# Kernel optimization log

Measured on AMD Instinct MI355X. Metric: run time of the kernel, lower is better.

The kernel has to match this reference:

```python
import jax, jax.numpy as jnp
import numpy as np

D = 1024       # total one-hot domain width
N = 65536      # number of synthetic records
N_ATTRS = 64   # attributes
BIN = 16       # categories per attribute (equal-size bins: N_ATTRS * BIN == D)
Q = 2048       # number of queries
K = 3          # k-way marginals


def setup_inputs() -> dict:
    key = jax.random.key(0)
    k1, k2 = jax.random.split(key)
    # UnifInitializer: (rand - 0.5) * 2 -> uniform in [-1, 1]
    weight = (jax.random.uniform(k1, (D, N), dtype=jnp.float32) - 0.5) * 2.0
    q_idxs = jax.random.randint(k2, (Q, K), 0, D)  # int query column indices into d
    return {"weight": weight, "q_idxs": q_idxs}


def reference(weight, q_idxs):
    # x = syndata.weight.T : [n, d]
    x = weight.T
    # _get_probs: per-attribute-bin softmax along d. Equal bins -> reshape+softmax.
    probs = jax.nn.softmax(x.reshape(N, N_ATTRS, BIN), axis=-1).reshape(N, D)
    # get_answers: gather query columns, product over k, mean over records.
    gathered = probs[:, q_idxs]          # [n, Q, k]
    answers = gathered.prod(axis=-1).mean(axis=0)  # [Q]
    return answers
```

## Files before the change

### kernel.cpp

```cpp
#include <hip/hip_runtime.h>
#include <stdint.h>

#define D_DIM 1024
#define N_DIM 65536
#define Q_DIM 2048
#define K_DIM 3

#define NBLK  256
#define TPB   1024
#define MACW  32
#define NMAC  8
#define NQT   32
#define QROWS 256

#define RING_OFF  0
#define TAB_OFF   98304
#define LDS_TOTAL 163840

#define VMCNT2() asm volatile("s_waitcnt vmcnt(2)" ::: "memory")
#define VMCNT0() asm volatile("s_waitcnt vmcnt(0)" ::: "memory")
#define LGKM0()  asm volatile("s_waitcnt lgkmcnt(0)" ::: "memory")
#define SCHED0() __builtin_amdgcn_sched_barrier(0)
#define SBAR()   __builtin_amdgcn_s_barrier()

typedef const __attribute__((address_space(1))) uint32_t  glb_u32;
typedef __attribute__((address_space(3))) uint32_t        lds_u32;

__device__ __forceinline__ uint32_t f2bf(float f) {
    uint32_t u = __float_as_uint(f);
    return (u + 0x7fffu + ((u >> 16) & 1u)) >> 16;
}
__device__ __forceinline__ float blo(uint32_t u) { return __uint_as_float(u << 16); }
__device__ __forceinline__ float bhi(uint32_t u) { return __uint_as_float(u & 0xffff0000u); }

__device__ __forceinline__ void stage_quarter(const float* __restrict__ W, char* smem,
                                              int q, int bid, int w, int l) {
    const int slot = (q % 3) * 32768;
    const int col0 = bid * (NMAC * MACW) + (q >> 2) * MACW;
    const int r0   = (q & 3) * QROWS + w * 16 + (l >> 3);
    const float* g0 = W + ((size_t)r0 << 16) + col0 + (l & 7) * 4;
    const float* g1 = W + ((size_t)(r0 + 8) << 16) + col0 + (l & 7) * 4;
    __builtin_amdgcn_global_load_lds((glb_u32*)g0, (lds_u32*)(smem + RING_OFF + slot + w * 2048 + l * 16),        16, 0, 0);
    __builtin_amdgcn_global_lds:
    ;
}

#undef RING_OFF
#define RING_OFF 0

__device__ __forceinline__ void stage_quarter2(const float* __restrict__ W, char* smem,
                                               int q, int bid, int w, int l) {
    const int slot = (q % 3) * 32768;
    const int col0 = bid * (NMAC * MACW) + (q >> 2) * MACW;
    const int r0   = (q & 3) * QROWS + w * 16 + (l >> 3);
    const float* g0 = W + ((size_t)r0 << 16) + col0 + (l & 7) * 4;
    const float* g1 = W + ((size_t)(r0 + 8) << 16) + col0 + (l & 7) * 4;
    __builtin_amdgcn_global_load_lds((glb_u32*)g0,
        (lds_u32*)(smem + RING_OFF + slot + w * 2048 + l * 16), 16, 0, 0);
    __builtin_amdgcn_global_load_lds((glb_u32*)g1,
        (lds_u32*)(smem + RING_OFF + slot + w * 2048 + 1024 + l * 16), 16, 0, 0);
}

#define COMPUTE_PHASE()                                                                           \
    _Pragma("unroll")                                                                             \
    for (int g16 = 0; g16 < 4; ++g16) {                                                           \
        const int gb = g16 << 4;                                                                  \
        {                                                                                         \
            const uint4 va = *(const uint4*)(smem + TAB_OFF + baseb[0][0] + (gb ^ swzb[0][0]));   \
            const uint4 vb = *(const uint4*)(smem + TAB_OFF + baseb[0][1] + (gb ^ swzb[0][1]));   \
            const uint4 vc = *(const uint4*)(smem + TAB_OFF + baseb[0][2] + (gb ^ swzb[0][2]));   \
            acc0 = fmaf(blo(va.x) * blo(vb.x), blo(vc.x), acc0);                                  \
            acc0 = fmaf(bhi(va.x) * bhi(vb.x), bhi(vc.x), acc0);                                  \
            acc0 = fmaf(blo(va.y) * blo(vb.y), blo(vc.y), acc0);                                  \
            acc0 = fmaf(bhi(va.y) * bhi(vb.y), bhi(vc.y), acc0);                                  \
            acc0 = fmaf(blo(va.z) * blo(vb.z), blo(vc.z), acc0);                                  \
            acc0 = fmaf(bhi(va.z) * bhi(vb.z), bhi(vc.z), acc0);                                  \
            acc0 = fmaf(blo(va.w) * blo(vb.w), blo(vc.w), acc0);                                  \
            acc0 = fmaf(bhi(va.w) * bhi(vb.w), bhi(vc.w), acc0);                                  \
        }                                                                                         \
        {                                                                                         \
            const uint4 va = *(const uint4*)(smem + TAB_OFF + baseb[1][0] + (gb ^ swzb[1][0]));   \
            const uint4 vb = *(const uint4*)(smem + TAB_OFF + baseb[1][1] + (gb ^ swzb[1][1]));   \
            const uint4 vc = *(const uint4*)(smem + TAB_OFF + baseb[1][2] + (gb ^ swzb[1][2]));   \
            acc1 = fmaf(blo(va.x) * blo(vb.x), blo(vc.x), acc1);                                  \
            acc1 = fmaf(bhi(va.x) * bhi(vb.x), bhi(vc.x), acc1);                                  \
            acc1 = fmaf(blo(va.y) * blo(vb.y), blo(vc.y), acc1);                                  \
            acc1 = fmaf(bhi(va.y) * bhi(vb.y), bhi(vc.y), acc1);                                  \
            acc1 = fmaf(blo(va.z) * blo(vb.z), blo(vc.z), acc1);                                  \
            acc1 = fmaf(bhi(va.z) * bhi(vb.z), bhi(vc.z), acc1);                                  \
            acc1 = fmaf(blo(va.w) * blo(vb.w), blo(vc.w), acc1);                                  \
            acc1 = fmaf(bhi(va.w) * bhi(vb.w), bhi(vc.w), acc1);                                  \
        }                                                                                         \
    }

template<bool ATOMIC>
__global__ __launch_bounds__(TPB, 4) void rap_main(const float* __restrict__ W,
                                                   const int* __restrict__ qidx,
                                                   float* __restrict__ outp) {
    extern __shared__ char smem[];
    const int tid = threadIdx.x;
    const int bid = blockIdx.x;
    const int w = tid >> 6, l = tid & 63;

    const int q0 = tid * 2;
    int baseb[2][K_DIM];
    int swzb[2][K_DIM];
#pragma unroll
    for (int qq = 0; qq < 2; ++qq) {
#pragma unroll
        for (int k = 0; k < K_DIM; ++k) {
            const int d = qidx[(q0 + qq) * K_DIM + k];
            baseb[qq][k] = d << 6;
            swzb[qq][k]  = ((d >> 1) & 3) << 4;
        }
    }

    const int c = l & 31;
    const int h = l >> 5;

    float acc0 = 0.f, acc1 = 0.f;

    VMCNT0(); SCHED0();
    stage_quarter2(W, smem, 0, bid, w, l);
    stage_quarter2(W, smem, 1, bid, w, l);

    for (int m = 0; m < NMAC; ++m) {
#pragma unroll
        for (int s = 0; s < 4; ++s) {
            const int q = m * 4 + s;
            if (q == NQT - 1) { VMCNT0(); } else { VMCNT2(); }
            SCHED0();

            if (q + 2 < NQT) stage_quarter2(W, smem, q + 2, bid, w, l);
            SCHED0();

            {
                const char* p = smem + RING_OFF + (q % 3) * 32768
                                + (w * 16 + h) * 128 + c * 4;
                float e[8]; float sum = 0.f;
#pragma unroll
                for (int j = 0; j < 8; ++j) {
                    e[j] = __expf(*(const float*)(p + j * 256));
                    sum += e[j];
                }
                sum += __shfl_xor(sum, 32);
                const float rec = __builtin_amdgcn_rcpf(sum);
                const int rbase = s * 256 + w * 16 + h;
#pragma unroll
                for (int j = 0; j < 8; ++j) {
                    const int row = rbase + 2 * j;
                    const uint32_t bf = f2bf(e[j] * rec);
                    *(uint16_t*)(smem + TAB_OFF + row * 64
                                 + ((((c >> 3) ^ ((row >> 1) & 3))) << 4)
                                 + ((c & 7) << 1)) = (uint16_t)bf;
                }
            }
        }

        LGKM0(); SCHED0(); SBAR(); SCHED0();

        COMPUTE_PHASE();

        LGKM0(); SCHED0(); SBAR(); SCHED0();
    }

    if (ATOMIC) {
        atomicAdd(outp + q0,     acc0 * (1.0f / N_DIM));
        atomicAdd(outp + q0 + 1, acc1 * (1.0f / N_DIM));
    } else {
        outp[(size_t)q0 * NBLK + bid]       = acc0;
        outp[(size_t)(q0 + 1) * NBLK + bid] = acc1;
    }
}

__global__ __launch_bounds__(256) void rap_reduce(const float* __restrict__ partials,
                                                  float* __restrict__ outp) {
    const int wv = threadIdx.x >> 6;
    const int l  = threadIdx.x & 63;
    const int qb = blockIdx.x * 8 + wv * 2;
#pragma unroll
    for (int i = 0; i < 2; ++i) {
        const int q = qb + i;
        const float* p = partials + (size_t)q * NBLK;
        float s = p[l] + p[l + 64] + p[l + 128] + p[l + 192];
        s += __shfl_xor(s, 1);
        s += __shfl_xor(s, 2);
        s += __shfl_xor(s, 4);
        s += __shfl_xor(s, 8);
        s += __shfl_xor(s, 16);
        s += __shfl_xor(s, 32);
        if (l == 0) outp[q] = s * (1.0f / N_DIM);
    }
}

extern "C" void kernel_launch(void* const* d_in, const int* in_sizes, int n_in,
                              void* d_out, int out_size, void* d_ws, size_t ws_size,
                              hipStream_t stream) {
    const float* W    = (const float*)d_in[0];
    const int*   qidx = (const int*)d_in[1];
    float*       outp = (float*)d_out;

    const size_t need = (size_t)Q_DIM * NBLK * sizeof(float);
    if (ws_size >= need) {
        (void)hipFuncSetAttribute((const void*)rap_main<false>,
                                  hipFuncAttributeMaxDynamicSharedMemorySize, LDS_TOTAL);
        float* partials = (float*)d_ws;
        hipLaunchKernelGGL(rap_main<false>, dim3(NBLK), dim3(TPB), LDS_TOTAL, stream,
                           W, qidx, partials);
        hipLaunchKernelGGL(rap_reduce, dim3(Q_DIM / 8), dim3(256), 0, stream,
                           partials, outp);
    } else {
        (void)hipFuncSetAttribute((const void*)rap_main<true>,
                                  hipFuncAttributeMaxDynamicSharedMemorySize, LDS_TOTAL);
        (void)hipMemsetAsync(d_out, 0, Q_DIM * sizeof(float), stream);
        hipLaunchKernelGGL(rap_main<true>, dim3(NBLK), dim3(TPB), LDS_TOTAL, stream,
                           W, qidx, outp);
    }
}
```

Measured before the change: 66.16 us.

## Store softmax table as custom 8-bit floats and deepen load ring to four slots

Replaces the bf16 probability table in LDS with a custom 8-bit float format (3 mantissa bits, scaled by 64), halving table size and the LDS bytes read per query triple. The freed LDS lets the global-to-LDS staging ring grow from three to four slots with a prefetch distance of three, and the vmcnt waits are adjusted to match. The final scaling folds the 64^3 factor into the mean. Much lower precision of the probabilities risks accuracy-tolerance failures, and the custom decode costs extra ALU work per element.

```diff
diff --git a/kernel.cpp b/kernel.cpp
--- a/kernel.cpp
+++ b/kernel.cpp
@@ -14,9 +14,11 @@
 #define QROWS 256
 
 #define RING_OFF  0
-#define TAB_OFF   98304
+#define TAB_OFF   131072
 #define LDS_TOTAL 163840
 
+#define VMCNT6() asm volatile("s_waitcnt vmcnt(6)" ::: "memory")
+#define VMCNT4() asm volatile("s_waitcnt vmcnt(4)" ::: "memory")
 #define VMCNT2() asm volatile("s_waitcnt vmcnt(2)" ::: "memory")
 #define VMCNT0() asm volatile("s_waitcnt vmcnt(0)" ::: "memory")
 #define LGKM0()  asm volatile("s_waitcnt lgkmcnt(0)" ::: "memory")
@@ -26,31 +28,16 @@
 typedef const __attribute__((address_space(1))) uint32_t  glb_u32;
 typedef __attribute__((address_space(3))) uint32_t        lds_u32;
 
-__device__ __forceinline__ uint32_t f2bf(float f) {
-    uint32_t u = __float_as_uint(f);
-    return (u + 0x7fffu + ((u >> 16) & 1u)) >> 16;
-}
-__device__ __forceinline__ float blo(uint32_t u) { return __uint_as_float(u << 16); }
-__device__ __forceinline__ float bhi(uint32_t u) { return __uint_as_float(u & 0xffff0000u); }
+__device__ __forceinline__ uint32_t f2fp8(float x) {
+    uint32_t u = __float_as_uint(x);
+    u += 0x7FFFFu + ((u >> 20) & 1u);
+    return (u >> 20) - 960u;
+}
+#define DEC(b) __uint_as_float(((b) + 960u) << 20)
 
 __device__ __forceinline__ void stage_quarter(const float* __restrict__ W, char* smem,
                                               int q, int bid, int w, int l) {
-    const int slot = (q % 3) * 32768;
-    const int col0 = bid * (NMAC * MACW) + (q >> 2) * MACW;
-    const int r0   = (q & 3) * QROWS + w * 16 + (l >> 3);
-    const float* g0 = W + ((size_t)r0 << 16) + col0 + (l & 7) * 4;
-    const float* g1 = W + ((size_t)(r0 + 8) << 16) + col0 + (l & 7) * 4;
-    __builtin_amdgcn_global_load_lds((glb_u32*)g0, (lds_u32*)(smem + RING_OFF + slot + w * 2048 + l * 16),        16, 0, 0);
-    __builtin_amdgcn_global_lds:
-    ;
-}
-
-#undef RING_OFF
-#define RING_OFF 0
-
-__device__ __forceinline__ void stage_quarter2(const float* __restrict__ W, char* smem,
-                                               int q, int bid, int w, int l) {
-    const int slot = (q % 3) * 32768;
+    const int slot = (q & 3) << 15;
     const int col0 = bid * (NMAC * MACW) + (q >> 2) * MACW;
     const int r0   = (q & 3) * QROWS + w * 16 + (l >> 3);
     const float* g0 = W + ((size_t)r0 << 16) + col0 + (l & 7) * 4;
@@ -61,36 +48,32 @@
         (lds_u32*)(smem + RING_OFF + slot + w * 2048 + 1024 + l * 16), 16, 0, 0);
 }
 
-#define COMPUTE_PHASE()                                                                           \
-    _Pragma("unroll")                                                                             \
-    for (int g16 = 0; g16 < 4; ++g16) {                                                           \
-        const int gb = g16 << 4;                                                                  \
-        {                                                                                         \
-            const uint4 va = *(const uint4*)(smem + TAB_OFF + baseb[0][0] + (gb ^ swzb[0][0]));   \
-            const uint4 vb = *(const uint4*)(smem + TAB_OFF + baseb[0][1] + (gb ^ swzb[0][1]));   \
-            const uint4 vc = *(const uint4*)(smem + TAB_OFF + baseb[0][2] + (gb ^ swzb[0][2]));   \
-            acc0 = fmaf(blo(va.x) * blo(vb.x), blo(vc.x), acc0);                                  \
-            acc0 = fmaf(bhi(va.x) * bhi(vb.x), bhi(vc.x), acc0);                                  \
-            acc0 = fmaf(blo(va.y) * blo(vb.y), blo(vc.y), acc0);                                  \
-            acc0 = fmaf(bhi(va.y) * bhi(vb.y), bhi(vc.y), acc0);                                  \
-            acc0 = fmaf(blo(va.z) * blo(vb.z), blo(vc.z), acc0);                                  \
-            acc0 = fmaf(bhi(va.z) * bhi(vb.z), bhi(vc.z), acc0);                                  \
-            acc0 = fmaf(blo(va.w) * blo(vb.w), blo(vc.w), acc0);                                  \
-            acc0 = fmaf(bhi(va.w) * bhi(vb.w), bhi(vc.w), acc0);                                  \
-        }                                                                                         \
-        {                                                                                         \
-            const uint4 va = *(const uint4*)(smem + TAB_OFF + baseb[1][0] + (gb ^ swzb[1][0]));   \
-            const uint4 vb = *(const uint4*)(smem + TAB_OFF + baseb[1][1] + (gb ^ swzb[1][1]));   \
-            const uint4 vc = *(const uint4*)(smem + TAB_OFF + baseb[1][2] + (gb ^ swzb[1][2]));   \
-            acc1 = fmaf(blo(va.x) * blo(vb.x), blo(vc.x), acc1);                                  \
-            acc1 = fmaf(bhi(va.x) * bhi(vb.x), bhi(vc.x), acc1);                                  \
-            acc1 = fmaf(blo(va.y) * blo(vb.y), blo(vc.y), acc1);                                  \
-            acc1 = fmaf(bhi(va.y) * bhi(vb.y), bhi(vc.y), acc1);                                  \
-            acc1 = fmaf(blo(va.z) * blo(vb.z), blo(vc.z), acc1);                                  \
-            acc1 = fmaf(bhi(va.z) * bhi(vb.z), bhi(vc.z), acc1);                                  \
-            acc1 = fmaf(blo(va.w) * blo(vb.w), blo(vc.w), acc1);                                  \
-            acc1 = fmaf(bhi(va.w) * bhi(vb.w), bhi(vc.w), acc1);                                  \
-        }                                                                                         \
+#define TRIPLE(va, vb, vc, sh, acc)                                                   \
+    acc = fmaf(DEC(((va) >> (sh)) & 0xFFu) * DEC(((vb) >> (sh)) & 0xFFu),             \
+               DEC(((vc) >> (sh)) & 0xFFu), acc)
+
+#define COMPUTE_PHASE()                                                               \
+    _Pragma("unroll")                                                                 \
+    for (int g16 = 0; g16 < 4; ++g16) {                                               \
+        const int gb = g16 << 3;                                                      \
+        _Pragma("unroll")                                                             \
+        for (int qq2 = 0; qq2 < 2; ++qq2) {                                           \
+            const uint2 va = *(const uint2*)(smem + TAB_OFF + baseb[qq2][0]           \
+                                             + (gb ^ swzb[qq2][0]));                  \
+            const uint2 vb = *(const uint2*)(smem + TAB_OFF + baseb[qq2][1]           \
+                                             + (gb ^ swzb[qq2][1]));                  \
+            const uint2 vc = *(const uint2*)(smem + TAB_OFF + baseb[qq2][2]           \
+                                             + (gb ^ swzb[qq2][2]));                  \
+            float& acc = qq2 ? acc1 : acc0;                                           \
+            TRIPLE(va.x, vb.x, vc.x, 0, acc);                                         \
+            TRIPLE(va.x, vb.x, vc.x, 8, acc);                                         \
+            TRIPLE(va.x, vb.x, vc.x, 16, acc);                                        \
+            TRIPLE(va.x, vb.x, vc.x, 24, acc);                                        \
+            TRIPLE(va.y, vb.y, vc.y, 0, acc);                                         \
+            TRIPLE(va.y, vb.y, vc.y, 8, acc);                                         \
+            TRIPLE(va.y, vb.y, vc.y, 16, acc);                                        \
+            TRIPLE(va.y, vb.y, vc.y, 24, acc);                                        \
+        }                                                                             \
     }
 
 template<bool ATOMIC>
@@ -110,8 +93,8 @@
 #pragma unroll
         for (int k = 0; k < K_DIM; ++k) {
             const int d = qidx[(q0 + qq) * K_DIM + k];
-            baseb[qq][k] = d << 6;
-            swzb[qq][k]  = ((d >> 1) & 3) << 4;
+            baseb[qq][k] = d << 5;
+            swzb[qq][k]  = ((d >> 1) & 3) << 3;
         }
     }
 
@@ -121,21 +104,27 @@
     float acc0 = 0.f, acc1 = 0.f;
 
     VMCNT0(); SCHED0();
-    stage_quarter2(W, smem, 0, bid, w, l);
-    stage_quarter2(W, smem, 1, bid, w, l);
+    stage_quarter(W, smem, 0, bid, w, l);
+    stage_quarter(W, smem, 1, bid, w, l);
+    stage_quarter(W, smem, 2, bid, w, l);
 
     for (int m = 0; m < NMAC; ++m) {
 #pragma unroll
         for (int s = 0; s < 4; ++s) {
             const int q = m * 4 + s;
-            if (q == NQT - 1) { VMCNT0(); } else { VMCNT2(); }
+
+            if (q + 3 < NQT) stage_quarter(W, smem, q + 3, bid, w, l);
             SCHED0();
 
-            if (q + 2 < NQT) stage_quarter2(W, smem, q + 2, bid, w, l);
+            const int rem = (NQT - 1) - q;
+            if (rem >= 3)      { VMCNT6(); }
+            else if (rem == 2) { VMCNT4(); }
+            else if (rem == 1) { VMCNT2(); }
+            else               { VMCNT0(); }
             SCHED0();
 
             {
-                const char* p = smem + RING_OFF + (q % 3) * 32768
+                const char* p = smem + RING_OFF + ((q & 3) << 15)
                                 + (w * 16 + h) * 128 + c * 4;
                 float e[8]; float sum = 0.f;
 #pragma unroll
@@ -144,15 +133,14 @@
                     sum += e[j];
                 }
                 sum += __shfl_xor(sum, 32);
-                const float rec = __builtin_amdgcn_rcpf(sum);
-                const int rbase = s * 256 + w * 16 + h;
+                const float rec64 = __builtin_amdgcn_rcpf(sum) * 64.0f;
+                const int rbase = (q & 3) * 256 + w * 16 + h;
 #pragma unroll
                 for (int j = 0; j < 8; ++j) {
                     const int row = rbase + 2 * j;
-                    const uint32_t bf = f2bf(e[j] * rec);
-                    *(uint16_t*)(smem + TAB_OFF + row * 64
-                                 + ((((c >> 3) ^ ((row >> 1) & 3))) << 4)
-                                 + ((c & 7) << 1)) = (uint16_t)bf;
+                    *(uint8_t*)(smem + TAB_OFF + row * 32
+                                + ((((c >> 3) ^ ((row >> 1) & 3))) << 3)
+                                + (c & 7)) = (uint8_t)f2fp8(e[j] * rec64);
                 }
             }
         }
@@ -165,8 +153,8 @@
     }
 
     if (ATOMIC) {
-        atomicAdd(outp + q0,     acc0 * (1.0f / N_DIM));
-        atomicAdd(outp + q0 + 1, acc1 * (1.0f / N_DIM));
+        atomicAdd(outp + q0,     acc0 * (1.0f / 17179869184.0f));
+        atomicAdd(outp + q0 + 1, acc1 * (1.0f / 17179869184.0f));
     } else {
         outp[(size_t)q0 * NBLK + bid]       = acc0;
         outp[(size_t)(q0 + 1) * NBLK + bid] = acc1;
@@ -189,7 +177,7 @@
         s += __shfl_xor(s, 8);
         s += __shfl_xor(s, 16);
         s += __shfl_xor(s, 32);
-        if (l == 0) outp[q] = s * (1.0f / N_DIM);
+        if (l == 0) outp[q] = s * (1.0f / 17179869184.0f);
     }
 }
 
```

After: 74.34 us. 1.12x slower.
